# Optimization experiments

Hardware: AMD Instinct MI355X
Metric: run time of the kernel (lower is better)

## Reference

```python
import jax, jax.numpy as jnp
import numpy as np

N_NODES = 50000
N_EDGES = 800000
C_IN = 128
C_OUT = 128


def setup_inputs() -> dict:
    key = jax.random.key(0)
    k1, k2, k3, k4 = jax.random.split(key, 4)
    x = jax.random.normal(k1, (N_NODES, C_IN), dtype=jnp.float32)
    edge_index = jax.random.randint(k2, (2, N_EDGES), 0, N_NODES, dtype=jnp.int64)
    # Linear(in, out): weight [out, in], bias [out]
    W = jax.random.normal(k3, (C_OUT, C_IN), dtype=jnp.float32) * (1.0 / np.sqrt(C_IN))
    b = jax.random.normal(k4, (C_OUT,), dtype=jnp.float32) * 0.01
    return {"x": x, "edge_index": edge_index, "W": W, "b": b}


def reference(x, edge_index, W, b):
    # GCN layer: out = D^{-1/2} (A + I) D^{-1/2} x W^T + b
    # Implemented as sparse gather/segment-sum (same math as the dense
    # adjacency matmul in the original, without the O(N^2) blowup).
    n = x.shape[0]
    loops = jnp.arange(n, dtype=edge_index.dtype)
    row = jnp.concatenate([edge_index[0], loops])  # [E+N]
    col = jnp.concatenate([edge_index[1], loops])  # [E+N]
    # degree over col index (as in pyg_utils.degree(edge_index[1], ...))
    ones = jnp.ones(row.shape[0], dtype=x.dtype)
    deg = jax.ops.segment_sum(ones, col, num_segments=n)
    deg_inv_sqrt = jnp.where(deg > 0, jax.lax.rsqrt(deg), 0.0).astype(x.dtype)
    norm = deg_inv_sqrt[row] * deg_inv_sqrt[col]  # [E+N]
    # aggregate: out[i] = sum_{(i,j) in edges} norm * x[j]
    msgs = x[col] * norm[:, None]  # [E+N, C_in]
    agg = jax.ops.segment_sum(msgs, row, num_segments=n)  # [N, C_in]
    return agg @ W.T + b
```

## Files before the change

kernel.cpp:

```cpp
#include <hip/hip_runtime.h>
#include <hip/hip_bf16.h>
#include <hip/hip_fp16.h>

#define C 128
#define NCH 32768
#define CN 2
#define CNODES (CN * NCH)
#define BE 64

typedef _Float16 f16x8 __attribute__((ext_vector_type(8)));
typedef _Float16 f16x4 __attribute__((ext_vector_type(4)));
typedef float f32x4 __attribute__((ext_vector_type(4)));

__global__ __launch_bounds__(256) void k_hist(
        const int* __restrict__ row, const int* __restrict__ col,
        unsigned char* __restrict__ part_row, unsigned char* __restrict__ part_col,
        unsigned char* __restrict__ tag, int E,
        __half* __restrict__ Z16, unsigned* __restrict__ gbase, int n) {
    __shared__ unsigned lh[NCH / 4];
    int bid = blockIdx.x;
    int tid = threadIdx.x;
    if (bid >= 2 * CN * BE) {
        if (tid < 16) {
            int pass = tid >> 3, g = tid & 7;
            ((uint4*)(Z16 + ((size_t)pass * (n + 1) + n) * 64))[g] =
                make_uint4(0u, 0u, 0u, 0u);
        }
        if (tid == 16) *gbase = 0u;
        return;
    }
    int side = (bid >= CN * BE) ? 1 : 0;
    int lb = side ? bid - CN * BE : bid;
    int c = lb >> 6;
    int b = lb & (BE - 1);
    for (int i = tid * 4; i < NCH / 4; i += 1024) {
        lh[i] = 0u; lh[i + 1] = 0u; lh[i + 2] = 0u; lh[i + 3] = 0u;
    }
    __syncthreads();
    int EPB = (E + BE - 1) / BE;
    int base = b * EPB;
    int end = min(base + EPB, E);
    const int* src = side ? col : row;

#define PROC_ROW(rv, ev)                                                  \
    if (((unsigned)(rv) >> 15) == (unsigned)c) {                          \
        int loc = (rv) & (NCH - 1);                                       \
        unsigned sh = ((unsigned)loc & 3u) << 3;                          \
        unsigned old = atomicAdd(&lh[loc >> 2], 1u << sh);                \
        tag[ev] = (unsigned char)((old >> sh) & 0xffu);                   \
    }
#define PROC_COL(rv)                                                      \
    if (((unsigned)(rv) >> 15) == (unsigned)c) {                          \
        int loc = (rv) & (NCH - 1);                                       \
        atomicAdd(&lh[loc >> 2], 1u << (((unsigned)loc & 3u) << 3));      \
    }
    int nv = 0;
    if ((((uintptr_t)(src + base)) & 15) == 0) nv = (end - base) >> 2;
    const int4* src4 = (const int4*)(src + base);
    if (!side) {
        for (int it = tid; it < nv; it += 256) {
            int4 v = src4[it];
            int e0 = base + it * 4;
            PROC_ROW(v.x, e0);
            PROC_ROW(v.y, e0 + 1);
            PROC_ROW(v.z, e0 + 2);
            PROC_ROW(v.w, e0 + 3);
        }
        for (int e = base + nv * 4 + tid; e < end; e += 256) {
            int r = src[e];
            PROC_ROW(r, e);
        }
    } else {
        for (int it = tid; it < nv; it += 256) {
            int4 v = src4[it];
            PROC_COL(v.x);
            PROC_COL(v.y);
            PROC_COL(v.z);
            PROC_COL(v.w);
        }
        for (int e = base + nv * 4 + tid; e < end; e += 256) {
            int r = src[e];
            PROC_COL(r);
        }
    }
#undef PROC_ROW
#undef PROC_COL
    __syncthreads();
    unsigned* dst = (unsigned*)((side ? part_col : part_row) + (size_t)b * CNODES + c * NCH);
    for (int i = tid; i < NCH / 4; i += 256) dst[i] = lh[i];
}

__global__ __launch_bounds__(256) void k_reduce_scan(
        unsigned char* __restrict__ part_row, const unsigned char* __restrict__ part_col,
        unsigned* __restrict__ start, unsigned* __restrict__ pcnt,
        unsigned* __restrict__ gbase, float* __restrict__ dis,
        int* __restrict__ scol, int n) {
    __shared__ unsigned s[256];
    __shared__ unsigned base_sh;
    int t = threadIdx.x;
    int i = blockIdx.x * 256 + t;
    unsigned acc = 0;
    if (i < n) {
#pragma unroll 8
        for (int b = 0; b < BE; ++b) {
            size_t off = (size_t)b * CNODES + i;
            unsigned v = part_row[off];
            part_row[off] = (unsigned char)acc;
            acc += v;
        }
        unsigned d = 0;
#pragma unroll 8
        for (int b = 0; b < BE; ++b) d += part_col[(size_t)b * CNODES + i];
        dis[i] = rsqrtf((float)(d + 1u));
    }
    unsigned v = (i < n) ? ((acc + 15u) & ~15u) : 0u;
    s[t] = v;
    __syncthreads();
    for (int off = 1; off < 256; off <<= 1) {
        unsigned add = (t >= off) ? s[t - off] : 0u;
        __syncthreads();
        s[t] += add;
        __syncthreads();
    }
    if (t == 255) base_sh = atomicAdd(gbase, s[255]);
    __syncthreads();
    if (i < n) {
        unsigned sb = base_sh + s[t] - v;
        start[i] = sb;
        pcnt[i] = v;
        for (unsigned k = acc; k < v; ++k) scol[sb + k] = n;
    }
}

__global__ __launch_bounds__(256) void k_scatter_gemm(
        const int* __restrict__ row, const int* __restrict__ col,
        const unsigned char* __restrict__ tag, const unsigned char* __restrict__ boff,
        const unsigned* __restrict__ start, int* __restrict__ scol, int E, int SB,
        const float* __restrict__ A, const float* __restrict__ W,
        const float* __restrict__ dis, __half* __restrict__ Z16, int n) {
    __shared__ char lds[128 * 256];
    int bid = blockIdx.x;
    int tid = threadIdx.x;
    if (bid < SB) {
        int e = bid * 256 + tid;
        if (e < E) {
            int EPB = (E + BE - 1) / BE;
            unsigned b = (unsigned)e / (unsigned)EPB;
            int r = row[e];
            unsigned p = start[r] + boff[(size_t)b * CNODES + r] + tag[e];
            scol[p] = col[e];
        }
        return;
    }
    int w = tid >> 6, lane = tid & 63;
    int m0 = (bid - SB) * 64;

#pragma unroll
    for (int i = 0; i < 16; ++i) {
        int fidx = i * 256 + tid;
        int nr = fidx >> 5;
        int c4 = fidx & 31;
        float4 wv = *(const float4*)(W + (size_t)nr * C + c4 * 4);
        f16x4 hh = {(_Float16)wv.x, (_Float16)wv.y, (_Float16)wv.z, (_Float16)wv.w};
        unsigned byte = (unsigned)(nr * 256 + c4 * 8);
        byte ^= (unsigned)((nr & 7) << 4);
        *(f16x4*)(lds + byte) = hh;
    }
    __syncthreads();

    int q = lane >> 4, rl = lane & 15;
    int r = m0 + w * 16 + rl;
    float dm = (r < n) ? dis[r] : 0.f;
    f32x4 acc[8] = {};
#pragma unroll
    for (int kc = 0; kc < 4; ++kc) {
        f16x8 af;
        float4 x0 = make_float4(0.f, 0.f, 0.f, 0.f), x1 = x0;
        if (r < n) {
            const float* srcx = A + (size_t)r * C + kc * 32 + q * 8;
            x0 = *(const float4*)srcx;
            x1 = *(const float4*)(srcx + 4);
        }
        af[0] = (_Float16)(x0.x * dm);
        af[1] = (_Float16)(x0.y * dm);
        af[2] = (_Float16)(x0.z * dm);
        af[3] = (_Float16)(x0.w * dm);
        af[4] = (_Float16)(x1.x * dm);
        af[5] = (_Float16)(x1.y * dm);
        af[6] = (_Float16)(x1.z * dm);
        af[7] = (_Float16)(x1.w * dm);
#pragma unroll
        for (int nt = 0; nt < 8; ++nt) {
            int nrow = nt * 16 + rl;
            unsigned byte = (unsigned)(nrow * 256 + kc * 64 + q * 16);
            byte ^= (unsigned)((nrow & 7) << 4);
            f16x8 bf = *(f16x8*)(lds + byte);
            acc[nt] = __builtin_amdgcn_mfma_f32_16x16x32_f16(af, bf, acc[nt], 0, 0, 0);
        }
    }
    __syncthreads();

#pragma unroll
    for (int nt = 0; nt < 8; ++nt)
#pragma unroll
        for (int i = 0; i < 4; ++i) {
            int row_l = w * 16 + q * 4 + i;
            int colh = nt * 16 + rl;
            unsigned byte = (unsigned)(row_l * 256 + colh * 2);
            byte ^= (unsigned)((row_l & 7) << 4);
            *(_Float16*)(lds + byte) = (_Float16)acc[nt][i];
        }
    __syncthreads();

#pragma unroll
    for (int it = 0; it < 4; ++it) {
        int idx = it * 256 + tid;
        int row_l = idx >> 4, c8 = idx & 15;
        unsigned byte = (unsigned)(row_l * 256 + c8 * 16);
        byte ^= (unsigned)((row_l & 7) << 4);
        uint4 v = *(uint4*)(lds + byte);
        int gr = m0 + row_l;
        if (gr < n) {
            int pass = c8 >> 3;
            int g = c8 & 7;
            *(uint4*)(Z16 + ((size_t)pass * (n + 1) + gr) * 64 + g * 8) = v;
        }
    }
}

__device__ __forceinline__ void add8(uint4 v, float2& a0, float2& a1,
                                     float2& a2, float2& a3) {
    float2 f;
    f = __half22float2(*(__half2*)&v.x); a0.x += f.x; a0.y += f.y;
    f = __half22float2(*(__half2*)&v.y); a1.x += f.x; a1.y += f.y;
    f = __half22float2(*(__half2*)&v.z); a2.x += f.x; a2.y += f.y;
    f = __half22float2(*(__half2*)&v.w); a3.x += f.x; a3.y += f.y;
}

__global__ __launch_bounds__(256) void k_agg(const __half* __restrict__ Z16,
                                             const int* __restrict__ scol,
                                             const unsigned* __restrict__ start,
                                             const unsigned* __restrict__ pcnt,
                                             const float* __restrict__ dis,
                                             const float* __restrict__ bias,
                                             float* __restrict__ out, int n, int RPB) {
    int bid = blockIdx.x;
    int pass = (bid >= RPB) ? 1 : 0;
    int rb = bid - pass * RPB;
    int wid = threadIdx.x >> 6;
    int lane = threadIdx.x & 63;
    int rw = lane >> 5;
    int slot = (lane >> 3) & 3;
    int g = lane & 7;
    int r = rb * 8 + wid * 2 + rw;
    if (r >= n) return;
    unsigned s0 = start[r];
    unsigned s1 = s0 + pcnt[r];
    float dr = dis[r];
    const uint4* Z4 = (const uint4*)(Z16 + (size_t)pass * (n + 1) * 64);
    float2 a0 = {0.f, 0.f}, a1 = a0, a2 = a0, a3 = a0;
    if (slot == 0) {
        uint4 v = Z4[(size_t)r * 8 + g];
        add8(v, a0, a1, a2, a3);
    }
    for (unsigned k = s0; k < s1; k += 16) {
        int c0 = scol[k + slot];
        int c1 = scol[k + 4 + slot];
        int c2 = scol[k + 8 + slot];
        int c3 = scol[k + 12 + slot];
        uint4 v0 = Z4[(size_t)c0 * 8 + g];
        uint4 v1 = Z4[(size_t)c1 * 8 + g];
        uint4 v2 = Z4[(size_t)c2 * 8 + g];
        uint4 v3 = Z4[(size_t)c3 * 8 + g];
        add8(v0, a0, a1, a2, a3);
        add8(v1, a0, a1, a2, a3);
        add8(v2, a0, a1, a2, a3);
        add8(v3, a0, a1, a2, a3);
    }
    a0.x += __shfl_xor(a0.x, 8);  a0.y += __shfl_xor(a0.y, 8);
    a1.x += __shfl_xor(a1.x, 8);  a1.y += __shfl_xor(a1.y, 8);
    a2.x += __shfl_xor(a2.x, 8);  a2.y += __shfl_xor(a2.y, 8);
    a3.x += __shfl_xor(a3.x, 8);  a3.y += __shfl_xor(a3.y, 8);
    a0.x += __shfl_xor(a0.x, 16); a0.y += __shfl_xor(a0.y, 16);
    a1.x += __shfl_xor(a1.x, 16); a1.y += __shfl_xor(a1.y, 16);
    a2.x += __shfl_xor(a2.x, 16); a2.y += __shfl_xor(a2.y, 16);
    a3.x += __shfl_xor(a3.x, 16); a3.y += __shfl_xor(a3.y, 16);
    if (slot == 0) {
        const float* bp = bias + pass * 64 + g * 8;
        float4 b0 = *(const float4*)bp;
        float4 b1 = *(const float4*)(bp + 4);
        float4 o0, o1;
        o0.x = b0.x + dr * a0.x; o0.y = b0.y + dr * a0.y;
        o0.z = b0.z + dr * a1.x; o0.w = b0.w + dr * a1.y;
        o1.x = b1.x + dr * a2.x; o1.y = b1.y + dr * a2.y;
        o1.z = b1.z + dr * a3.x; o1.w = b1.w + dr * a3.y;
        float* op = out + (size_t)r * C + pass * 64 + g * 8;
        *(float4*)op = o0;
        *(float4*)(op + 4) = o1;
    }
}

extern "C" void kernel_launch(void* const* d_in, const int* in_sizes, int n_in,
                              void* d_out, int out_size, void* d_ws, size_t ws_size,
                              hipStream_t stream) {
    const float* x  = (const float*)d_in[0];
    const int*   ei = (const int*)d_in[1];
    const float* W  = (const float*)d_in[2];
    const float* b  = (const float*)d_in[3];
    float* out = (float*)d_out;

    int n = in_sizes[0] / C;
    int E = in_sizes[1] / 2;
    const int* row = ei;
    const int* col = ei + E;

    char* p = (char*)d_ws;
    size_t cap  = (size_t)E + 15 * (size_t)n;
    size_t sz_part = (((size_t)BE * CNODES) + 511) & ~(size_t)511;
    size_t sz_n    = (((size_t)n * 4) + 511) & ~(size_t)511;
    size_t sz_E1   = (((size_t)E) + 511) & ~(size_t)511;
    size_t sz_cap  = ((cap * 4) + 511) & ~(size_t)511;
    size_t off = 0;
    unsigned char*  part_row = (unsigned char*)(p + off);  off += sz_part;
    unsigned char*  part_col = (unsigned char*)(p + off);  off += sz_part;
    unsigned*       start    = (unsigned*)(p + off);       off += sz_n;
    unsigned*       pcnt     = (unsigned*)(p + off);       off += sz_n;
    float*          dis      = (float*)(p + off);          off += sz_n;
    unsigned*       gbase    = (unsigned*)(p + off);       off += 512;
    unsigned char*  tag      = (unsigned char*)(p + off);  off += sz_E1;
    int*            scol     = (int*)(p + off);            off += sz_cap;
    __half*         z16      = (__half*)(p + off);

    int NT = 256;
    int NB = (n + NT - 1) / NT;
    int SB = (E + NT - 1) / NT;
    int GB = (n + 63) / 64;
    int RPB = (n + 7) / 8;

    k_hist<<<2 * CN * BE + 1, NT, 0, stream>>>(row, col, part_row, part_col, tag, E,
                                               z16, gbase, n);
    k_reduce_scan<<<NB, NT, 0, stream>>>(part_row, part_col, start, pcnt, gbase, dis,
                                         scol, n);
    k_scatter_gemm<<<SB + GB, NT, 0, stream>>>(row, col, tag, part_row, start, scol,
                                               E, SB, x, W, dis, z16, n);
    k_agg<<<2 * RPB, NT, 0, stream>>>(z16, scol, start, pcnt, dis, b, out, n, RPB);
}
```

Before: 77.15 us.

## Fuse scan with GEMM, recompute degrees in GEMM, double histogram partitions

Result: no change. 76.75 us (-0.5%).

```diff
diff --git a/kernel.cpp b/kernel.cpp
--- a/kernel.cpp
+++ b/kernel.cpp
@@ -6,7 +6,7 @@
 #define NCH 32768
 #define CN 2
 #define CNODES (CN * NCH)
-#define BE 64
+#define BE 128
 
 typedef _Float16 f16x8 __attribute__((ext_vector_type(8)));
 typedef _Float16 f16x4 __attribute__((ext_vector_type(4)));
@@ -15,7 +15,7 @@
 __global__ __launch_bounds__(256) void k_hist(
         const int* __restrict__ row, const int* __restrict__ col,
         unsigned char* __restrict__ part_row, unsigned char* __restrict__ part_col,
-        unsigned char* __restrict__ tag, int E,
+        unsigned char* __restrict__ tag, int E, int EPB,
         __half* __restrict__ Z16, unsigned* __restrict__ gbase, int n) {
     __shared__ unsigned lh[NCH / 4];
     int bid = blockIdx.x;
@@ -31,13 +31,12 @@
     }
     int side = (bid >= CN * BE) ? 1 : 0;
     int lb = side ? bid - CN * BE : bid;
-    int c = lb >> 6;
+    int c = lb >> 7;
     int b = lb & (BE - 1);
     for (int i = tid * 4; i < NCH / 4; i += 1024) {
         lh[i] = 0u; lh[i + 1] = 0u; lh[i + 2] = 0u; lh[i + 3] = 0u;
     }
     __syncthreads();
-    int EPB = (E + BE - 1) / BE;
     int base = b * EPB;
     int end = min(base + EPB, E);
     const int* src = side ? col : row;
@@ -54,8 +53,7 @@
         int loc = (rv) & (NCH - 1);                                       \
         atomicAdd(&lh[loc >> 2], 1u << (((unsigned)loc & 3u) << 3));      \
     }
-    int nv = 0;
-    if ((((uintptr_t)(src + base)) & 15) == 0) nv = (end - base) >> 2;
+    int nv = (end > base) ? ((end - base) >> 2) : 0;
     const int4* src4 = (const int4*)(src + base);
     if (!side) {
         for (int it = tid; it < nv; it += 256) {
@@ -90,70 +88,58 @@
     for (int i = tid; i < NCH / 4; i += 256) dst[i] = lh[i];
 }
 
-__global__ __launch_bounds__(256) void k_reduce_scan(
+__global__ __launch_bounds__(256) void k_scan_gemm(
         unsigned char* __restrict__ part_row, const unsigned char* __restrict__ part_col,
         unsigned* __restrict__ start, unsigned* __restrict__ pcnt,
         unsigned* __restrict__ gbase, float* __restrict__ dis,
-        int* __restrict__ scol, int n) {
-    __shared__ unsigned s[256];
-    __shared__ unsigned base_sh;
-    int t = threadIdx.x;
-    int i = blockIdx.x * 256 + t;
-    unsigned acc = 0;
-    if (i < n) {
-#pragma unroll 8
-        for (int b = 0; b < BE; ++b) {
-            size_t off = (size_t)b * CNODES + i;
-            unsigned v = part_row[off];
-            part_row[off] = (unsigned char)acc;
-            acc += v;
-        }
-        unsigned d = 0;
-#pragma unroll 8
-        for (int b = 0; b < BE; ++b) d += part_col[(size_t)b * CNODES + i];
-        dis[i] = rsqrtf((float)(d + 1u));
-    }
-    unsigned v = (i < n) ? ((acc + 15u) & ~15u) : 0u;
-    s[t] = v;
-    __syncthreads();
-    for (int off = 1; off < 256; off <<= 1) {
-        unsigned add = (t >= off) ? s[t - off] : 0u;
-        __syncthreads();
-        s[t] += add;
-        __syncthreads();
-    }
-    if (t == 255) base_sh = atomicAdd(gbase, s[255]);
-    __syncthreads();
-    if (i < n) {
-        unsigned sb = base_sh + s[t] - v;
-        start[i] = sb;
-        pcnt[i] = v;
-        for (unsigned k = acc; k < v; ++k) scol[sb + k] = n;
-    }
-}
-
-__global__ __launch_bounds__(256) void k_scatter_gemm(
-        const int* __restrict__ row, const int* __restrict__ col,
-        const unsigned char* __restrict__ tag, const unsigned char* __restrict__ boff,
-        const unsigned* __restrict__ start, int* __restrict__ scol, int E, int SB,
+        int* __restrict__ scol, int NB,
         const float* __restrict__ A, const float* __restrict__ W,
-        const float* __restrict__ dis, __half* __restrict__ Z16, int n) {
+        __half* __restrict__ Z16, int n) {
     __shared__ char lds[128 * 256];
     int bid = blockIdx.x;
     int tid = threadIdx.x;
-    if (bid < SB) {
-        int e = bid * 256 + tid;
-        if (e < E) {
-            int EPB = (E + BE - 1) / BE;
-            unsigned b = (unsigned)e / (unsigned)EPB;
-            int r = row[e];
-            unsigned p = start[r] + boff[(size_t)b * CNODES + r] + tag[e];
-            scol[p] = col[e];
+
+    if (bid < NB) {
+        unsigned* s = (unsigned*)lds;
+        unsigned* base_sh = (unsigned*)(lds + 1024);
+        int t = tid;
+        int i = bid * 256 + t;
+        unsigned acc = 0;
+        if (i < n) {
+#pragma unroll 8
+            for (int b = 0; b < BE; ++b) {
+                size_t off = (size_t)b * CNODES + i;
+                unsigned v = part_row[off];
+                part_row[off] = (unsigned char)acc;
+                acc += v;
+            }
+            unsigned d = 0;
+#pragma unroll 8
+            for (int b = 0; b < BE; ++b) d += part_col[(size_t)b * CNODES + i];
+            dis[i] = rsqrtf((float)(d + 1u));
+        }
+        unsigned v = (i < n) ? ((acc + 15u) & ~15u) : 0u;
+        s[t] = v;
+        __syncthreads();
+        for (int off = 1; off < 256; off <<= 1) {
+            unsigned add = (t >= off) ? s[t - off] : 0u;
+            __syncthreads();
+            s[t] += add;
+            __syncthreads();
+        }
+        if (t == 255) *base_sh = atomicAdd(gbase, s[255]);
+        __syncthreads();
+        if (i < n) {
+            unsigned sb = *base_sh + s[t] - v;
+            start[i] = sb;
+            pcnt[i] = v;
+            for (unsigned k = acc; k < v; ++k) scol[sb + k] = n;
         }
         return;
     }
+
     int w = tid >> 6, lane = tid & 63;
-    int m0 = (bid - SB) * 64;
+    int m0 = (bid - NB) * 64;
 
 #pragma unroll
     for (int i = 0; i < 16; ++i) {
@@ -166,11 +152,18 @@
         byte ^= (unsigned)((nr & 7) << 4);
         *(f16x4*)(lds + byte) = hh;
     }
-    __syncthreads();
 
     int q = lane >> 4, rl = lane & 15;
     int r = m0 + w * 16 + rl;
-    float dm = (r < n) ? dis[r] : 0.f;
+    unsigned d = 0;
+#pragma unroll 8
+    for (int j = 0; j < BE / 4; ++j)
+        d += part_col[(size_t)(q * (BE / 4) + j) * CNODES + r];
+    d += (unsigned)__shfl_xor((int)d, 16);
+    d += (unsigned)__shfl_xor((int)d, 32);
+    float dm = (r < n) ? rsqrtf((float)(d + 1u)) : 0.f;
+    __syncthreads();
+
     f32x4 acc[8] = {};
 #pragma unroll
     for (int kc = 0; kc < 4; ++kc) {
@@ -225,6 +218,19 @@
             int g = c8 & 7;
             *(uint4*)(Z16 + ((size_t)pass * (n + 1) + gr) * 64 + g * 8) = v;
         }
+    }
+}
+
+__global__ __launch_bounds__(256) void k_scatter(
+        const int* __restrict__ row, const int* __restrict__ col,
+        const unsigned char* __restrict__ tag, const unsigned char* __restrict__ boff,
+        const unsigned* __restrict__ start, int* __restrict__ scol, int E, int EPB) {
+    int e = blockIdx.x * 256 + threadIdx.x;
+    if (e < E) {
+        unsigned b = (unsigned)e / (unsigned)EPB;
+        int r = row[e];
+        unsigned p = start[r] + boff[(size_t)b * CNODES + r] + tag[e];
+        scol[p] = col[e];
     }
 }
 
@@ -333,15 +339,15 @@
 
     int NT = 256;
     int NB = (n + NT - 1) / NT;
+    int EPB = (((E + BE - 1) / BE) + 3) & ~3;
     int SB = (E + NT - 1) / NT;
     int GB = (n + 63) / 64;
     int RPB = (n + 7) / 8;
 
     k_hist<<<2 * CN * BE + 1, NT, 0, stream>>>(row, col, part_row, part_col, tag, E,
-                                               z16, gbase, n);
-    k_reduce_scan<<<NB, NT, 0, stream>>>(part_row, part_col, start, pcnt, gbase, dis,
-                                         scol, n);
-    k_scatter_gemm<<<SB + GB, NT, 0, stream>>>(row, col, tag, part_row, start, scol,
-                                               E, SB, x, W, dis, z16, n);
+                                               EPB, z16, gbase, n);
+    k_scan_gemm<<<NB + GB, NT, 0, stream>>>(part_row, part_col, start, pcnt, gbase,
+                                            dis, scol, NB, x, W, z16, n);
+    k_scatter<<<SB, NT, 0, stream>>>(row, col, tag, part_row, start, scol, E, EPB);
     k_agg<<<2 * RPB, NT, 0, stream>>>(z16, scol, start, pcnt, dis, b, out, n, RPB);
 }
```
